# Optimization experiments

Measured on AMD Instinct MI355X. Metric: run time of the kernel, lower is better.

Reference implementation:

```python
import jax, jax.numpy as jnp
import numpy as np

B, NF, FD = 2048, 64, 32   # batch, n_features, feature_dim
S = NF // 2                # n_sites
D, OD = 32, 32             # bond_dim, out_dim


def setup_inputs() -> dict:
    key = jax.random.key(0)
    k1, k2, k3, k4 = jax.random.split(key, 4)
    sc = 1.0 / np.sqrt(FD * D)
    x = jax.random.normal(k1, (B, NF, FD), dtype=jnp.float32)
    L = jax.random.normal(k2, (S, FD, D, D), dtype=jnp.float32) * sc
    R = jax.random.normal(k3, (S, FD, D, D), dtype=jnp.float32) * sc
    O = jax.random.normal(k4, (S, D, D, OD), dtype=jnp.float32) * sc
    bias = jnp.zeros((S, OD), dtype=jnp.float32)
    return {"x": x, "L": L, "R": R, "O": O, "bias": bias}


def reference(x, L, R, O, bias):
    # x: [B, 2*S, FD] -> left/right features per site
    xL = x[:, 0::2, :]  # [B, S, FD]
    xR = x[:, 1::2, :]  # [B, S, FD]
    # feature -> bond matrices
    A = jnp.einsum('bsf,sfam->bsam', xL, L)   # [B, S, D, D]
    Bm = jnp.einsum('bsg,sgan->bsan', xR, R)  # [B, S, D, D]
    # contract shared bond leg a, then output tensor
    M = jnp.einsum('bsam,bsan->bsmn', A, Bm)  # [B, S, D, D]
    out = jnp.einsum('bsmn,smno->bso', M, O)  # [B, S, OD]
    return out + bias  # bias broadcast over batch; activation is None
```

## Files before the change

kernel.cpp:

```cpp
#include <hip/hip_runtime.h>
#include <hip/hip_bf16.h>

typedef __attribute__((ext_vector_type(4)))  _Float16 h4;
typedef __attribute__((ext_vector_type(8)))  _Float16 h8;
typedef __attribute__((ext_vector_type(4)))  float f32x4;
typedef __attribute__((ext_vector_type(16))) float f32x16;
typedef __attribute__((ext_vector_type(4)))  unsigned int u32x4;

__device__ __forceinline__ int sdecode(int sp) { return ((sp & 7) << 2) | (sp >> 3); }

__global__ __launch_bounds__(64) void conv_kernel(
    const float* __restrict__ Rg, const float* __restrict__ Og,
    _Float16* __restrict__ Rb, char* __restrict__ Opp)
{
    __shared__ float tile[32][33];
    const int bid = blockIdx.x;
    const int s = sdecode(bid & 31), q = (bid >> 5) & 31, which = bid >> 10;
    const int t = threadIdx.x, tl = t & 31, th = t >> 5;

    if (which == 0) {
        #pragma unroll
        for (int j = 0; j < 16; ++j) {
            int ar = 2*j + th;
            tile[tl][ar] = Rg[(((size_t)s*32 + q)*32 + ar)*32 + tl];
        }
        __syncthreads();
        _Float16* dst = Rb + ((size_t)s*32 + q)*1024;
        #pragma unroll
        for (int it = 0; it < 4; ++it) {
            int nr = it*8 + (t >> 3), a0 = (t & 7)*4;
            h4 w;
            #pragma unroll
            for (int k = 0; k < 4; ++k) w[k] = (_Float16)tile[nr][a0 + k];
            *(h4*)(dst + nr*32 + a0) = w;
        }
    } else {
        #pragma unroll
        for (int j = 0; j < 16; ++j) {
            int nr = 2*j + th;
            tile[tl][nr] = Og[(((size_t)s*32 + q)*32 + nr)*32 + tl];
        }
        __syncthreads();
        char* dst = Opp + (size_t)s*65536 + q*2048;
        int o = t & 31, cq = t >> 5;
        #pragma unroll
        for (int it = 0; it < 2; ++it) {
            int c = it*2 + cq;
            h8 w;
            #pragma unroll
            for (int k = 0; k < 8; ++k) w[k] = (_Float16)tile[o][c*8 + k];
            *(h8*)(dst + c*512 + o*16) = w;
        }
    }
}

__global__ __launch_bounds__(256, 2) void tmake_kernel(
    const float* __restrict__ Lg, const _Float16* __restrict__ Rb,
    const char* __restrict__ Opp, char* __restrict__ Tp)
{
    __shared__ __align__(16) char Wl[65536];
    const int bid = blockIdx.x;
    const int s = sdecode(bid & 31), f = bid >> 5;
    const int t = threadIdx.x, wid = t >> 6, l = t & 63;
    const int llo = l & 15, lhi = l >> 4;

    const float* Lsf = Lg + ((size_t)s*32 + f)*1024;
    h8 bfr[2];
    #pragma unroll
    for (int mt = 0; mt < 2; ++mt)
        #pragma unroll
        for (int j = 0; j < 8; ++j)
            bfr[mt][j] = (_Float16)Lsf[(8*lhi + j)*32 + mt*16 + llo];

    const _Float16* Rbs = Rb + (size_t)s*32768;

    #pragma unroll 4
    for (int nt = 0; nt < 16; ++nt) {
        int gnb = (wid*16 + nt)*16;
        h8 af = *(const h8*)(Rbs + (gnb + llo)*32 + 8*lhi);
        int g = gnb >> 5;
        int nbase = (gnb & 31) + 4*lhi;
        #pragma unroll
        for (int mt = 0; mt < 2; ++mt) {
            f32x4 d = __builtin_amdgcn_mfma_f32_16x16x32_f16(af, bfr[mt], (f32x4)(0.f), 0, 0, 0);
            int m = mt*16 + llo;
            h4 w;
            #pragma unroll
            for (int r = 0; r < 4; ++r) w[r] = (_Float16)d[r];
            int byte = (g*2048 + m*64 + nbase*2) ^ ((((g & 7) ^ (m & 7))) << 4);
            *(h4*)(Wl + byte) = w;
        }
    }
    __syncthreads();

    const int ot = wid & 1, kq = wid >> 1;
    const int orow = ot*16 + llo;
    const char* Opps = Opp + (size_t)s*65536;
    f32x4 acc0 = (f32x4)(0.f), acc1 = (f32x4)(0.f);
    #pragma unroll 4
    for (int ksl = 0; ksl < 16; ++ksl) {
        int ks = kq*16 + ksl;
        h8 bf = *(const h8*)(Opps + (ks*4 + lhi)*512 + orow*16);
        {
            int grow = llo;
            int byte = (grow*2048 + ks*64 + lhi*16) ^ ((((grow & 7) ^ (ks & 7))) << 4);
            h8 af = *(const h8*)(Wl + byte);
            acc0 = __builtin_amdgcn_mfma_f32_16x16x32_f16(af, bf, acc0, 0, 0, 0);
        }
        {
            int grow = 16 + llo;
            int byte = (grow*2048 + ks*64 + lhi*16) ^ ((((grow & 7) ^ (ks & 7))) << 4);
            h8 af = *(const h8*)(Wl + byte);
            acc1 = __builtin_amdgcn_mfma_f32_16x16x32_f16(af, bf, acc1, 0, 0, 0);
        }
    }
    __syncthreads();
    if (kq == 1) {
        *(f32x4*)(Wl + ((ot*2 + 0)*64 + l)*16) = acc0;
        *(f32x4*)(Wl + ((ot*2 + 1)*64 + l)*16) = acc1;
    }
    __syncthreads();
    if (kq == 0) {
        acc0 += *(const f32x4*)(Wl + ((ot*2 + 0)*64 + l)*16);
        acc1 += *(const f32x4*)(Wl + ((ot*2 + 1)*64 + l)*16);
        char* Tps = Tp + (size_t)s*65536;
        h4 w0, w1;
        #pragma unroll
        for (int r = 0; r < 4; ++r) { w0[r] = (_Float16)acc0[r]; w1[r] = (_Float16)acc1[r]; }
        *(h4*)(Tps + (f*2 + 0)*1024 + orow*32 + lhi*8) = w0;
        *(h4*)(Tps + (f*2 + 1)*1024 + orow*32 + lhi*8) = w1;
    }
}

__global__ __launch_bounds__(512, 2) void main_kernel(
    const float* __restrict__ x, const char* __restrict__ Tp,
    const float* __restrict__ bias, float* __restrict__ out)
{
    __shared__ __align__(16) char Tl[65536];

    const int bid = blockIdx.x;
    const int s = sdecode(bid & 31);
    const int b0 = (bid >> 5) * 256;
    const int t = threadIdx.x, wid = t >> 6, l = t & 63;
    const int lo5 = l & 31, hi = l >> 5;

    const char* Tps = Tp + (size_t)s*65536;
    const float* xrow = x + (size_t)(b0 + wid*32 + lo5)*2048 + s*64;
    const float* bias_s = bias + s*32;

    u32x4 tv[8];
    #pragma unroll
    for (int i = 0; i < 8; ++i)
        tv[i] = *(const u32x4*)(Tps + (i*512 + t)*16);

    float4 xlv[8];
    #pragma unroll
    for (int i = 0; i < 8; ++i) xlv[i] = *(const float4*)(xrow + i*4);
    const float* xrp = xrow + 32 + hi*8;
    float4 xr00 = *(const float4*)(xrp);
    float4 xr01 = *(const float4*)(xrp + 4);
    float4 xr10 = *(const float4*)(xrp + 16);
    float4 xr11 = *(const float4*)(xrp + 20);

    #pragma unroll
    for (int i = 0; i < 8; ++i)
        *(u32x4*)(Tl + (i*512 + t)*16) = tv[i];

    h4 xlh[8];
    #pragma unroll
    for (int i = 0; i < 8; ++i) {
        xlh[i][0] = (_Float16)xlv[i].x; xlh[i][1] = (_Float16)xlv[i].y;
        xlh[i][2] = (_Float16)xlv[i].z; xlh[i][3] = (_Float16)xlv[i].w;
    }
    h8 xr_a, xr_b;
    xr_a[0] = (_Float16)xr00.x; xr_a[1] = (_Float16)xr00.y;
    xr_a[2] = (_Float16)xr00.z; xr_a[3] = (_Float16)xr00.w;
    xr_a[4] = (_Float16)xr01.x; xr_a[5] = (_Float16)xr01.y;
    xr_a[6] = (_Float16)xr01.z; xr_a[7] = (_Float16)xr01.w;
    xr_b[0] = (_Float16)xr10.x; xr_b[1] = (_Float16)xr10.y;
    xr_b[2] = (_Float16)xr10.z; xr_b[3] = (_Float16)xr10.w;
    xr_b[4] = (_Float16)xr11.x; xr_b[5] = (_Float16)xr11.y;
    xr_b[6] = (_Float16)xr11.z; xr_b[7] = (_Float16)xr11.w;
    __syncthreads();

    f32x16 acc_e = (f32x16)(0.f), acc_o = (f32x16)(0.f);
    #pragma unroll
    for (int ksl = 0; ksl < 64; ++ksl) {
        h8 bf = *(const h8*)(Tl + ksl*1024 + lo5*32 + hi*16);
        _Float16 xs = xlh[ksl >> 3][(ksl >> 1) & 3];
        if (ksl & 1) {
            h8 z = xr_b * xs;
            acc_o = __builtin_amdgcn_mfma_f32_32x32x16_f16(z, bf, acc_o, 0, 0, 0);
        } else {
            h8 z = xr_a * xs;
            acc_e = __builtin_amdgcn_mfma_f32_32x32x16_f16(z, bf, acc_e, 0, 0, 0);
        }
    }
    f32x16 acc = acc_e + acc_o;

    __syncthreads();
    #pragma unroll
    for (int r = 0; r < 16; ++r) {
        int row = (r & 3) + 8*(r >> 2) + 4*hi;
        *(float*)(Tl + wid*4096 + row*128 + lo5*4) = acc[r];
    }
    __syncthreads();

    #pragma unroll
    for (int i = 0; i < 4; ++i) {
        int u = i*512 + t;
        int row = u >> 3, colq = u & 7;
        f32x4 v = *(const f32x4*)(Tl + u*16);
        f32x4 bv = *(const f32x4*)(bias_s + colq*4);
        *(f32x4*)(out + (size_t)(b0 + row)*1024 + s*32 + colq*4) = v + bv;
    }
}

extern "C" void kernel_launch(void* const* d_in, const int* in_sizes, int n_in,
                              void* d_out, int out_size, void* d_ws, size_t ws_size,
                              hipStream_t stream) {
    const float* x    = (const float*)d_in[0];
    const float* L    = (const float*)d_in[1];
    const float* R    = (const float*)d_in[2];
    const float* O    = (const float*)d_in[3];
    const float* bias = (const float*)d_in[4];
    float* out = (float*)d_out;

    _Float16* Rb  = (_Float16*)d_ws;
    char*     Opp = (char*)d_ws + 2097152;
    char*     Tp  = (char*)d_ws + 4194304;

    conv_kernel<<<dim3(2048), 64, 0, stream>>>(R, O, Rb, Opp);
    tmake_kernel<<<dim3(1024), 256, 0, stream>>>(L, Rb, Opp, Tp);
    main_kernel<<<dim3(256), 512, 0, stream>>>(x, Tp, bias, out);
}
```

Baseline: 30.54 us.

## Pre-transpose x to site-major fp16 and add output transpose kernel

The prep kernel now packs four R/O conversion tiles per 256-thread block and also converts x to fp16 in a site-major layout, so main_kernel reads contiguous 128-byte rows instead of strided fp32 rows. main_kernel writes results site-major to a workspace buffer, and a new outtrans kernel adds bias and transposes through LDS to write the final output with coalesced stores. This is meant to remove uncoalesced global access in the main kernel. In exchange it adds an extra kernel launch and roughly 8 MB of additional workspace traffic in each direction.

```diff
diff --git a/kernel.cpp b/kernel.cpp
--- a/kernel.cpp
+++ b/kernel.cpp
@@ -9,47 +9,75 @@
 
 __device__ __forceinline__ int sdecode(int sp) { return ((sp & 7) << 2) | (sp >> 3); }
 
-__global__ __launch_bounds__(64) void conv_kernel(
+__global__ __launch_bounds__(256) void prep_kernel(
     const float* __restrict__ Rg, const float* __restrict__ Og,
-    _Float16* __restrict__ Rb, char* __restrict__ Opp)
-{
-    __shared__ float tile[32][33];
-    const int bid = blockIdx.x;
-    const int s = sdecode(bid & 31), q = (bid >> 5) & 31, which = bid >> 10;
-    const int t = threadIdx.x, tl = t & 31, th = t >> 5;
-
-    if (which == 0) {
-        #pragma unroll
-        for (int j = 0; j < 16; ++j) {
-            int ar = 2*j + th;
-            tile[tl][ar] = Rg[(((size_t)s*32 + q)*32 + ar)*32 + tl];
+    const float* __restrict__ x,
+    _Float16* __restrict__ Rb, char* __restrict__ Opp, char* __restrict__ xh)
+{
+    __shared__ float tiles[4][32][34];
+    const int bid = blockIdx.x;
+    const int t = threadIdx.x, wid = t >> 6, l = t & 63;
+
+    if (bid < 512) {
+        const int obid = bid*4 + wid;
+        const int s = sdecode(obid & 31), q = (obid >> 5) & 31, which = obid >> 10;
+        float (*tile)[34] = tiles[wid];
+        const int tl = l & 31, th = l >> 5;
+
+        if (which == 0) {
+            #pragma unroll
+            for (int j = 0; j < 16; ++j) {
+                int ar = 2*j + th;
+                tile[tl][ar] = Rg[(((size_t)s*32 + q)*32 + ar)*32 + tl];
+            }
+        } else {
+            #pragma unroll
+            for (int j = 0; j < 16; ++j) {
+                int nr = 2*j + th;
+                tile[tl][nr] = Og[(((size_t)s*32 + q)*32 + nr)*32 + tl];
+            }
         }
         __syncthreads();
-        _Float16* dst = Rb + ((size_t)s*32 + q)*1024;
-        #pragma unroll
-        for (int it = 0; it < 4; ++it) {
-            int nr = it*8 + (t >> 3), a0 = (t & 7)*4;
-            h4 w;
-            #pragma unroll
-            for (int k = 0; k < 4; ++k) w[k] = (_Float16)tile[nr][a0 + k];
-            *(h4*)(dst + nr*32 + a0) = w;
+        if (which == 0) {
+            _Float16* dst = Rb + ((size_t)s*32 + q)*1024;
+            #pragma unroll
+            for (int it = 0; it < 4; ++it) {
+                int nr = it*8 + (l >> 3), a0 = (l & 7)*4;
+                h4 w;
+                #pragma unroll
+                for (int k = 0; k < 4; ++k) w[k] = (_Float16)tile[nr][a0 + k];
+                *(h4*)(dst + nr*32 + a0) = w;
+            }
+        } else {
+            char* dst = Opp + (size_t)s*65536 + q*2048;
+            int o = l & 31, cq = l >> 5;
+            #pragma unroll
+            for (int it = 0; it < 2; ++it) {
+                int c = it*2 + cq;
+                h8 w;
+                #pragma unroll
+                for (int k = 0; k < 8; ++k) w[k] = (_Float16)tile[o][c*8 + k];
+                *(h8*)(dst + c*512 + o*16) = w;
+            }
         }
     } else {
-        #pragma unroll
-        for (int j = 0; j < 16; ++j) {
-            int nr = 2*j + th;
-            tile[tl][nr] = Og[(((size_t)s*32 + q)*32 + nr)*32 + tl];
-        }
-        __syncthreads();
-        char* dst = Opp + (size_t)s*65536 + q*2048;
-        int o = t & 31, cq = t >> 5;
-        #pragma unroll
-        for (int it = 0; it < 2; ++it) {
-            int c = it*2 + cq;
+        const int xbid = bid - 512;
+        const int b0x = xbid * 32;
+        const float* xb = x + (size_t)b0x * 2048;
+        #pragma unroll 4
+        for (int c = 0; c < 32; ++c) {
+            int g = c*256 + t;
+            float4 v0 = *(const float4*)(xb + (size_t)g*8);
+            float4 v1 = *(const float4*)(xb + (size_t)g*8 + 4);
             h8 w;
-            #pragma unroll
-            for (int k = 0; k < 8; ++k) w[k] = (_Float16)tile[o][c*8 + k];
-            *(h8*)(dst + c*512 + o*16) = w;
+            w[0] = (_Float16)v0.x; w[1] = (_Float16)v0.y;
+            w[2] = (_Float16)v0.z; w[3] = (_Float16)v0.w;
+            w[4] = (_Float16)v1.x; w[5] = (_Float16)v1.y;
+            w[6] = (_Float16)v1.z; w[7] = (_Float16)v1.w;
+            int row = g >> 8;
+            int s2 = (g & 255) >> 3;
+            int cf = (g & 7) * 8;
+            *(h8*)(xh + ((size_t)s2*2048 + b0x + row)*128 + cf*2) = w;
         }
     }
 }
@@ -133,8 +161,8 @@
 }
 
 __global__ __launch_bounds__(512, 2) void main_kernel(
-    const float* __restrict__ x, const char* __restrict__ Tp,
-    const float* __restrict__ bias, float* __restrict__ out)
+    const char* __restrict__ xh, const char* __restrict__ Tp,
+    char* __restrict__ outT)
 {
     __shared__ __align__(16) char Tl[65536];
 
@@ -145,49 +173,30 @@
     const int lo5 = l & 31, hi = l >> 5;
 
     const char* Tps = Tp + (size_t)s*65536;
-    const float* xrow = x + (size_t)(b0 + wid*32 + lo5)*2048 + s*64;
-    const float* bias_s = bias + s*32;
+    const int b = b0 + wid*32 + lo5;
+    const char* xrow = xh + ((size_t)s*2048 + b)*128;
 
     u32x4 tv[8];
     #pragma unroll
     for (int i = 0; i < 8; ++i)
         tv[i] = *(const u32x4*)(Tps + (i*512 + t)*16);
 
-    float4 xlv[8];
-    #pragma unroll
-    for (int i = 0; i < 8; ++i) xlv[i] = *(const float4*)(xrow + i*4);
-    const float* xrp = xrow + 32 + hi*8;
-    float4 xr00 = *(const float4*)(xrp);
-    float4 xr01 = *(const float4*)(xrp + 4);
-    float4 xr10 = *(const float4*)(xrp + 16);
-    float4 xr11 = *(const float4*)(xrp + 20);
+    h8 xlh8[4];
+    #pragma unroll
+    for (int i = 0; i < 4; ++i) xlh8[i] = *(const h8*)(xrow + i*16);
+    h8 xr_a = *(const h8*)(xrow + 64 + hi*16);
+    h8 xr_b = *(const h8*)(xrow + 96 + hi*16);
 
     #pragma unroll
     for (int i = 0; i < 8; ++i)
         *(u32x4*)(Tl + (i*512 + t)*16) = tv[i];
-
-    h4 xlh[8];
-    #pragma unroll
-    for (int i = 0; i < 8; ++i) {
-        xlh[i][0] = (_Float16)xlv[i].x; xlh[i][1] = (_Float16)xlv[i].y;
-        xlh[i][2] = (_Float16)xlv[i].z; xlh[i][3] = (_Float16)xlv[i].w;
-    }
-    h8 xr_a, xr_b;
-    xr_a[0] = (_Float16)xr00.x; xr_a[1] = (_Float16)xr00.y;
-    xr_a[2] = (_Float16)xr00.z; xr_a[3] = (_Float16)xr00.w;
-    xr_a[4] = (_Float16)xr01.x; xr_a[5] = (_Float16)xr01.y;
-    xr_a[6] = (_Float16)xr01.z; xr_a[7] = (_Float16)xr01.w;
-    xr_b[0] = (_Float16)xr10.x; xr_b[1] = (_Float16)xr10.y;
-    xr_b[2] = (_Float16)xr10.z; xr_b[3] = (_Float16)xr10.w;
-    xr_b[4] = (_Float16)xr11.x; xr_b[5] = (_Float16)xr11.y;
-    xr_b[6] = (_Float16)xr11.z; xr_b[7] = (_Float16)xr11.w;
     __syncthreads();
 
     f32x16 acc_e = (f32x16)(0.f), acc_o = (f32x16)(0.f);
     #pragma unroll
     for (int ksl = 0; ksl < 64; ++ksl) {
         h8 bf = *(const h8*)(Tl + ksl*1024 + lo5*32 + hi*16);
-        _Float16 xs = xlh[ksl >> 3][(ksl >> 1) & 3];
+        _Float16 xs = xlh8[ksl >> 4][(ksl >> 1) & 7];
         if (ksl & 1) {
             h8 z = xr_b * xs;
             acc_o = __builtin_amdgcn_mfma_f32_32x32x16_f16(z, bf, acc_o, 0, 0, 0);
@@ -211,8 +220,35 @@
         int u = i*512 + t;
         int row = u >> 3, colq = u & 7;
         f32x4 v = *(const f32x4*)(Tl + u*16);
-        f32x4 bv = *(const f32x4*)(bias_s + colq*4);
-        *(f32x4*)(out + (size_t)(b0 + row)*1024 + s*32 + colq*4) = v + bv;
+        *(f32x4*)(outT + ((size_t)s*2048 + b0 + row)*128 + colq*16) = v;
+    }
+}
+
+__global__ __launch_bounds__(256) void outtrans_kernel(
+    const char* __restrict__ outT, const float* __restrict__ bias,
+    float* __restrict__ out)
+{
+    __shared__ __align__(16) char lds[65536];
+    const int bid = blockIdx.x;
+    const int b0 = bid * 16;
+    const int t = threadIdx.x;
+
+    #pragma unroll
+    for (int sp2 = 0; sp2 < 16; ++sp2) {
+        int s = sp2*2 + (t >> 7);
+        int u = t & 127, row = u >> 3, colq = u & 7;
+        f32x4 v = *(const f32x4*)(outT + ((size_t)s*2048 + b0 + row)*128 + colq*16);
+        f32x4 bv = *(const f32x4*)(bias + s*32 + colq*4);
+        v = v + bv;
+        int cu = s*8 + (colq ^ (row & 7));
+        *(f32x4*)(lds + row*4096 + cu*16) = v;
+    }
+    __syncthreads();
+
+    #pragma unroll
+    for (int r2 = 0; r2 < 16; ++r2) {
+        f32x4 v = *(const f32x4*)(lds + r2*4096 + (t ^ (r2 & 7))*16);
+        *(f32x4*)(out + (size_t)(b0 + r2)*1024 + t*4) = v;
     }
 }
 
@@ -226,11 +262,14 @@
     const float* bias = (const float*)d_in[4];
     float* out = (float*)d_out;
 
-    _Float16* Rb  = (_Float16*)d_ws;
-    char*     Opp = (char*)d_ws + 2097152;
-    char*     Tp  = (char*)d_ws + 4194304;
-
-    conv_kernel<<<dim3(2048), 64, 0, stream>>>(R, O, Rb, Opp);
+    _Float16* Rb   = (_Float16*)d_ws;
+    char*     Opp  = (char*)d_ws + 2097152;
+    char*     Tp   = (char*)d_ws + 4194304;
+    char*     outT = (char*)d_ws + 6291456;
+    char*     xh   = (char*)d_ws + 14680064;
+
+    prep_kernel<<<dim3(576), 256, 0, stream>>>(R, O, x, Rb, Opp, xh);
     tmake_kernel<<<dim3(1024), 256, 0, stream>>>(L, Rb, Opp, Tp);
-    main_kernel<<<dim3(256), 512, 0, stream>>>(x, Tp, bias, out);
-}
+    main_kernel<<<dim3(256), 512, 0, stream>>>(xh, Tp, outT);
+    outtrans_kernel<<<dim3(128), 256, 0, stream>>>(outT, bias, out);
+}
```

Result: slower. 38.43 us (+25.8%).

## Precast x to fp16 site-major layout in tmake and halve main block size

Applied to the files above, without the earlier changes.

tmake_kernel now also converts x from fp32 to fp16 and scatters it into a per-site contiguous workspace buffer. main_kernel then reads compact fp16 rows instead of strided fp32 rows, and no longer converts in registers. main_kernel also moves from 256 blocks of 512 threads to 512 blocks of 128-batch tiles with 256 threads, which spreads the work over more CUs. The cost is an extra write and read of x through the workspace, and the extra conversion work added to tmake.

```diff
diff --git a/kernel.cpp b/kernel.cpp
--- a/kernel.cpp
+++ b/kernel.cpp
@@ -6,6 +6,8 @@
 typedef __attribute__((ext_vector_type(4)))  float f32x4;
 typedef __attribute__((ext_vector_type(16))) float f32x16;
 typedef __attribute__((ext_vector_type(4)))  unsigned int u32x4;
+
+#define XH_STRIDE 262400
 
 __device__ __forceinline__ int sdecode(int sp) { return ((sp & 7) << 2) | (sp >> 3); }
 
@@ -56,13 +58,31 @@
 
 __global__ __launch_bounds__(256, 2) void tmake_kernel(
     const float* __restrict__ Lg, const _Float16* __restrict__ Rb,
-    const char* __restrict__ Opp, char* __restrict__ Tp)
+    const char* __restrict__ Opp, char* __restrict__ Tp,
+    const float* __restrict__ x, char* __restrict__ xh)
 {
     __shared__ __align__(16) char Wl[65536];
     const int bid = blockIdx.x;
     const int s = sdecode(bid & 31), f = bid >> 5;
     const int t = threadIdx.x, wid = t >> 6, l = t & 63;
     const int llo = l & 15, lhi = l >> 4;
+
+    {
+        const int u0 = (bid*256 + t)*2;
+        #pragma unroll
+        for (int k = 0; k < 2; ++k) {
+            int u = u0 + k;
+            int b = u >> 8, pos = u & 255, s2 = pos >> 3, c = pos & 7;
+            float4 v0 = *(const float4*)(x + (size_t)u*8);
+            float4 v1 = *(const float4*)(x + (size_t)u*8 + 4);
+            h8 w;
+            w[0] = (_Float16)v0.x; w[1] = (_Float16)v0.y;
+            w[2] = (_Float16)v0.z; w[3] = (_Float16)v0.w;
+            w[4] = (_Float16)v1.x; w[5] = (_Float16)v1.y;
+            w[6] = (_Float16)v1.z; w[7] = (_Float16)v1.w;
+            *(h8*)(xh + (size_t)s2*XH_STRIDE + b*128 + c*16) = w;
+        }
+    }
 
     const float* Lsf = Lg + ((size_t)s*32 + f)*1024;
     h8 bfr[2];
@@ -132,62 +152,42 @@
     }
 }
 
-__global__ __launch_bounds__(512, 2) void main_kernel(
-    const float* __restrict__ x, const char* __restrict__ Tp,
+__global__ __launch_bounds__(256, 2) void main_kernel(
+    const char* __restrict__ xh, const char* __restrict__ Tp,
     const float* __restrict__ bias, float* __restrict__ out)
 {
     __shared__ __align__(16) char Tl[65536];
 
     const int bid = blockIdx.x;
     const int s = sdecode(bid & 31);
-    const int b0 = (bid >> 5) * 256;
+    const int b0 = (bid >> 5) * 128;
     const int t = threadIdx.x, wid = t >> 6, l = t & 63;
     const int lo5 = l & 31, hi = l >> 5;
 
     const char* Tps = Tp + (size_t)s*65536;
-    const float* xrow = x + (size_t)(b0 + wid*32 + lo5)*2048 + s*64;
-    const float* bias_s = bias + s*32;
-
-    u32x4 tv[8];
-    #pragma unroll
-    for (int i = 0; i < 8; ++i)
-        tv[i] = *(const u32x4*)(Tps + (i*512 + t)*16);
-
-    float4 xlv[8];
-    #pragma unroll
-    for (int i = 0; i < 8; ++i) xlv[i] = *(const float4*)(xrow + i*4);
-    const float* xrp = xrow + 32 + hi*8;
-    float4 xr00 = *(const float4*)(xrp);
-    float4 xr01 = *(const float4*)(xrp + 4);
-    float4 xr10 = *(const float4*)(xrp + 16);
-    float4 xr11 = *(const float4*)(xrp + 20);
-
-    #pragma unroll
-    for (int i = 0; i < 8; ++i)
-        *(u32x4*)(Tl + (i*512 + t)*16) = tv[i];
-
-    h4 xlh[8];
-    #pragma unroll
-    for (int i = 0; i < 8; ++i) {
-        xlh[i][0] = (_Float16)xlv[i].x; xlh[i][1] = (_Float16)xlv[i].y;
-        xlh[i][2] = (_Float16)xlv[i].z; xlh[i][3] = (_Float16)xlv[i].w;
-    }
-    h8 xr_a, xr_b;
-    xr_a[0] = (_Float16)xr00.x; xr_a[1] = (_Float16)xr00.y;
-    xr_a[2] = (_Float16)xr00.z; xr_a[3] = (_Float16)xr00.w;
-    xr_a[4] = (_Float16)xr01.x; xr_a[5] = (_Float16)xr01.y;
-    xr_a[6] = (_Float16)xr01.z; xr_a[7] = (_Float16)xr01.w;
-    xr_b[0] = (_Float16)xr10.x; xr_b[1] = (_Float16)xr10.y;
-    xr_b[2] = (_Float16)xr10.z; xr_b[3] = (_Float16)xr10.w;
-    xr_b[4] = (_Float16)xr11.x; xr_b[5] = (_Float16)xr11.y;
-    xr_b[6] = (_Float16)xr11.z; xr_b[7] = (_Float16)xr11.w;
+    const char* xrow = xh + (size_t)s*XH_STRIDE + (b0 + wid*32 + lo5)*128;
+
+    u32x4 tv[16];
+    #pragma unroll
+    for (int i = 0; i < 16; ++i)
+        tv[i] = *(const u32x4*)(Tps + (i*256 + t)*16);
+
+    h8 xlh8[4];
+    #pragma unroll
+    for (int i = 0; i < 4; ++i) xlh8[i] = *(const h8*)(xrow + i*16);
+    h8 xr_a = *(const h8*)(xrow + 64 + hi*16);
+    h8 xr_b = *(const h8*)(xrow + 96 + hi*16);
+
+    #pragma unroll
+    for (int i = 0; i < 16; ++i)
+        *(u32x4*)(Tl + (i*256 + t)*16) = tv[i];
     __syncthreads();
 
     f32x16 acc_e = (f32x16)(0.f), acc_o = (f32x16)(0.f);
     #pragma unroll
     for (int ksl = 0; ksl < 64; ++ksl) {
         h8 bf = *(const h8*)(Tl + ksl*1024 + lo5*32 + hi*16);
-        _Float16 xs = xlh[ksl >> 3][(ksl >> 1) & 3];
+        _Float16 xs = xlh8[ksl >> 4][(ksl >> 1) & 7];
         if (ksl & 1) {
             h8 z = xr_b * xs;
             acc_o = __builtin_amdgcn_mfma_f32_32x32x16_f16(z, bf, acc_o, 0, 0, 0);
@@ -206,9 +206,10 @@
     }
     __syncthreads();
 
+    const float* bias_s = bias + s*32;
     #pragma unroll
     for (int i = 0; i < 4; ++i) {
-        int u = i*512 + t;
+        int u = i*256 + t;
         int row = u >> 3, colq = u & 7;
         f32x4 v = *(const f32x4*)(Tl + u*16);
         f32x4 bv = *(const f32x4*)(bias_s + colq*4);
@@ -229,8 +230,9 @@
     _Float16* Rb  = (_Float16*)d_ws;
     char*     Opp = (char*)d_ws + 2097152;
     char*     Tp  = (char*)d_ws + 4194304;
+    char*     xh  = (char*)d_ws + 6291456;
 
     conv_kernel<<<dim3(2048), 64, 0, stream>>>(R, O, Rb, Opp);
-    tmake_kernel<<<dim3(1024), 256, 0, stream>>>(L, Rb, Opp, Tp);
-    main_kernel<<<dim3(256), 512, 0, stream>>>(x, Tp, bias, out);
-}
+    tmake_kernel<<<dim3(1024), 256, 0, stream>>>(L, Rb, Opp, Tp, x, xh);
+    main_kernel<<<dim3(512), 256, 0, stream>>>(xh, Tp, bias, out);
+}
```

After: 32.44 us. 6.2% more time.

## Process two adjacent sites per main-kernel block with 1024 threads

Applied to the files above, without the earlier changes.

The main kernel now gives each block a pair of adjacent sites (16 waves, 128 KB LDS) and halves the grid to 128 blocks. Each block staged T for both sites and writes full 64-float contiguous output spans per row, so output stores are wider and coalesced. The cost is fewer blocks (128 on a chip with more CUs), larger LDS per block and 1024-thread blocks, which may reduce occupancy and leave CUs idle. The launch bounds of (1024,4) cannot be met with 128 KB of LDS.

```diff
diff --git a/kernel.cpp b/kernel.cpp
--- a/kernel.cpp
+++ b/kernel.cpp
@@ -132,27 +132,36 @@
     }
 }
 
-__global__ __launch_bounds__(512, 2) void main_kernel(
+__global__ __launch_bounds__(1024, 4) void main_kernel(
     const float* __restrict__ x, const char* __restrict__ Tp,
     const float* __restrict__ bias, float* __restrict__ out)
 {
-    __shared__ __align__(16) char Tl[65536];
+    __shared__ __align__(16) char Tl[131072];
 
     const int bid = blockIdx.x;
-    const int s = sdecode(bid & 31);
-    const int b0 = (bid >> 5) * 256;
+    const int spair = bid & 15;
+    const int b0 = (bid >> 4) * 256;
     const int t = threadIdx.x, wid = t >> 6, l = t & 63;
     const int lo5 = l & 31, hi = l >> 5;
-
-    const char* Tps = Tp + (size_t)s*65536;
-    const float* xrow = x + (size_t)(b0 + wid*32 + lo5)*2048 + s*64;
-    const float* bias_s = bias + s*32;
-
-    u32x4 tv[8];
-    #pragma unroll
-    for (int i = 0; i < 8; ++i)
-        tv[i] = *(const u32x4*)(Tps + (i*512 + t)*16);
-
+    const int ws = wid >> 3, wloc = wid & 7;
+    const int s_w = spair*2 + ws;
+
+    {
+        const char* src = Tp + (size_t)(spair*2 + (t >> 9))*65536;
+        char* dst = Tl + (t >> 9)*65536;
+        const int tt = t & 511;
+        u32x4 tv[4];
+        #pragma unroll
+        for (int i = 0; i < 4; ++i) tv[i] = *(const u32x4*)(src + (i*512 + tt)*16);
+        #pragma unroll
+        for (int i = 0; i < 4; ++i) *(u32x4*)(dst + (i*512 + tt)*16) = tv[i];
+        #pragma unroll
+        for (int i = 0; i < 4; ++i) tv[i] = *(const u32x4*)(src + ((i + 4)*512 + tt)*16);
+        #pragma unroll
+        for (int i = 0; i < 4; ++i) *(u32x4*)(dst + ((i + 4)*512 + tt)*16) = tv[i];
+    }
+
+    const float* xrow = x + (size_t)(b0 + wloc*32 + lo5)*2048 + s_w*64;
     float4 xlv[8];
     #pragma unroll
     for (int i = 0; i < 8; ++i) xlv[i] = *(const float4*)(xrow + i*4);
@@ -161,10 +170,6 @@
     float4 xr01 = *(const float4*)(xrp + 4);
     float4 xr10 = *(const float4*)(xrp + 16);
     float4 xr11 = *(const float4*)(xrp + 20);
-
-    #pragma unroll
-    for (int i = 0; i < 8; ++i)
-        *(u32x4*)(Tl + (i*512 + t)*16) = tv[i];
 
     h4 xlh[8];
     #pragma unroll
@@ -183,10 +188,11 @@
     xr_b[6] = (_Float16)xr11.z; xr_b[7] = (_Float16)xr11.w;
     __syncthreads();
 
+    const char* Tw = Tl + ws*65536;
     f32x16 acc_e = (f32x16)(0.f), acc_o = (f32x16)(0.f);
     #pragma unroll
     for (int ksl = 0; ksl < 64; ++ksl) {
-        h8 bf = *(const h8*)(Tl + ksl*1024 + lo5*32 + hi*16);
+        h8 bf = *(const h8*)(Tw + ksl*1024 + lo5*32 + hi*16);
         _Float16 xs = xlh[ksl >> 3][(ksl >> 1) & 3];
         if (ksl & 1) {
             h8 z = xr_b * xs;
@@ -201,18 +207,18 @@
     __syncthreads();
     #pragma unroll
     for (int r = 0; r < 16; ++r) {
-        int row = (r & 3) + 8*(r >> 2) + 4*hi;
-        *(float*)(Tl + wid*4096 + row*128 + lo5*4) = acc[r];
+        int row = wloc*32 + (r & 3) + 8*(r >> 2) + 4*hi;
+        *(float*)(Tl + row*256 + ws*128 + lo5*4) = acc[r];
     }
     __syncthreads();
 
     #pragma unroll
     for (int i = 0; i < 4; ++i) {
-        int u = i*512 + t;
-        int row = u >> 3, colq = u & 7;
+        int u = i*1024 + t;
+        int row = u >> 4, un = u & 15;
         f32x4 v = *(const f32x4*)(Tl + u*16);
-        f32x4 bv = *(const f32x4*)(bias_s + colq*4);
-        *(f32x4*)(out + (size_t)(b0 + row)*1024 + s*32 + colq*4) = v + bv;
+        f32x4 bv = *(const f32x4*)(bias + (spair*2 + (un >> 3))*32 + (un & 7)*4);
+        *(f32x4*)(out + (size_t)(b0 + row)*1024 + spair*64 + un*4) = v + bv;
     }
 }
 
@@ -232,5 +238,5 @@
 
     conv_kernel<<<dim3(2048), 64, 0, stream>>>(R, O, Rb, Opp);
     tmake_kernel<<<dim3(1024), 256, 0, stream>>>(L, Rb, Opp, Tp);
-    main_kernel<<<dim3(256), 512, 0, stream>>>(x, Tp, bias, out);
-}
+    main_kernel<<<dim3(128), 1024, 0, stream>>>(x, Tp, bias, out);
+}
```

After: 33.13 us. 8.5% more time.
